# Optimization experiments

Measured on AMD Instinct MI355X. Metric: run time of the kernel, lower is better.

The kernel has to match this reference:

```python
import jax, jax.numpy as jnp
import numpy as np

HID, HEADS, LAYERS = 64, 4, 2
D = HID // HEADS
NU, NE, NV = 30000, 60000, 1000
N_NODES = (NU, NE, NV)
OFFS = (0, NU, NU + NE, NU + NE + NV)
N_TOTAL = NU + NE + NV
# (src_type, dst_type, n_edges); node types: user=0, event=1, venue=2. Order matches module.edge_types.
EDGE_DEFS = (
    (0, 0, 150000),  # friend
    (0, 1, 120000), (0, 1, 60000), (0, 1, 40000), (0, 1, 30000), (0, 1, 50000),  # view/like/save/intent/attend
    (1, 0, 120000), (1, 0, 60000), (1, 0, 40000), (1, 0, 30000), (1, 0, 50000),  # rev_*
    (1, 2, 60000),  # hosted_at
    (2, 1, 60000),  # hosts
)
EDGE_NAMES = ('ei_friend', 'ei_view', 'ei_like', 'ei_save', 'ei_intent', 'ei_attend',
              'ei_rev_view', 'ei_rev_like', 'ei_rev_save', 'ei_rev_intent', 'ei_rev_attend',
              'ei_hosted_at', 'ei_hosts')


def _l2norm(x):
    return x / jnp.maximum(jnp.linalg.norm(x, axis=-1, keepdims=True), 1e-12)


def _hgt_layer(h, edges, Wkqv, bkqv, Wk, Wv, p_rel, Wout, bout, skip):
    # h: list of per-node-type features [N_t, HID]. Fused K/Q/V projection per node type.
    kqv = [h[t] @ Wkqv[t] + bkqv[t] for t in range(3)]  # [N_t, 3*HID]
    k = [a[:, :HID].reshape(-1, HEADS, D) for a in kqv]
    q = [a[:, HID:2 * HID].reshape(-1, HEADS, D) for a in kqv]
    v = [a[:, 2 * HID:].reshape(-1, HEADS, D) for a in kqv]
    scale = 1.0 / np.sqrt(D).astype(np.float32)
    scores, msgs, dsts = [], [], []
    for e, (s, d, _) in enumerate(EDGE_DEFS):
        src_idx, dst_idx = edges[e][0], edges[e][1]
        # per-(edge_type, head) DxD relation transforms (PyG k_rel / v_rel)
        ke = jnp.einsum('nhd,hde->nhe', k[s], Wk[e])[src_idx]  # [E,H,D]
        ve = jnp.einsum('nhd,hde->nhe', v[s], Wv[e])[src_idx]  # [E,H,D]
        qi = q[d][dst_idx]                                      # [E,H,D]
        scores.append((qi * ke).sum(-1) * p_rel[e] * scale)     # [E,H]
        msgs.append(ve)
        dsts.append(dst_idx + OFFS[d])
    sc = jnp.concatenate(scores)   # [E_tot, H]
    ms = jnp.concatenate(msgs)     # [E_tot, H, D]
    dst = jnp.concatenate(dsts)    # [E_tot] global destination ids
    # destination-grouped softmax across all edge types jointly
    smax = jax.lax.stop_gradient(jax.ops.segment_max(sc, dst, num_segments=N_TOTAL))
    ex = jnp.exp(sc - smax[dst])
    den = jax.ops.segment_sum(ex, dst, num_segments=N_TOTAL)
    alpha = ex / den[dst]
    agg = jax.ops.segment_sum(alpha[:, :, None] * ms, dst, num_segments=N_TOTAL).reshape(N_TOTAL, HID)
    out = []
    for t in range(3):
        o = agg[OFFS[t]:OFFS[t + 1]]
        a = jax.nn.gelu(o, approximate=False) @ Wout[t] + bout[t]
        g = jax.nn.sigmoid(skip[t])  # learnable skip gate
        out.append(g * a + (1.0 - g) * h[t])
    return out


def _forward(x_user, x_event, x_venue, W_user, b_user, W_event, b_event, W_venue, b_venue,
             emb_user, emb_event, emb_venue, Wkqv, bkqv, Wk, Wv, p_rel, Wout, bout, skip,
             ids_user, ids_event, ids_venue, edges):
    h = [x_user @ W_user + b_user + emb_user[ids_user],
         x_event @ W_event + b_event + emb_event[ids_event],
         x_venue @ W_venue + b_venue + emb_venue[ids_venue]]
    for l in range(LAYERS):
        h = _hgt_layer(h, edges, Wkqv[l], bkqv[l], Wk[l], Wv[l], p_rel[l], Wout[l], bout[l], skip[l])
        h = [jax.nn.relu(x) for x in h]  # dropout is identity in eval mode
    return tuple(_l2norm(x) for x in h)


def setup_inputs() -> dict:
    key = jax.random.key(0)
    ks = iter(jax.random.split(key, 64))
    s = 0.05
    inp = {
        'x_user': jax.random.normal(next(ks), (NU, 32), jnp.float32),
        'x_event': jax.random.normal(next(ks), (NE, 32), jnp.float32),
        'x_venue': jax.random.normal(next(ks), (NV, 16), jnp.float32),
        'W_user': jax.random.normal(next(ks), (32, HID), jnp.float32) * s,
        'b_user': jnp.zeros((HID,), jnp.float32),
        'W_event': jax.random.normal(next(ks), (32, HID), jnp.float32) * s,
        'b_event': jnp.zeros((HID,), jnp.float32),
        'W_venue': jax.random.normal(next(ks), (16, HID), jnp.float32) * s,
        'b_venue': jnp.zeros((HID,), jnp.float32),
        'emb_user': jax.random.normal(next(ks), (NU, HID), jnp.float32) * s,
        'emb_event': jax.random.normal(next(ks), (NE, HID), jnp.float32) * s,
        'emb_venue': jax.random.normal(next(ks), (NV, HID), jnp.float32) * s,
        'Wkqv': jax.random.normal(next(ks), (LAYERS, 3, HID, 3 * HID), jnp.float32) * s,
        'bkqv': jnp.zeros((LAYERS, 3, 3 * HID), jnp.float32),
        'Wk': jax.random.normal(next(ks), (LAYERS, 13, HEADS, D, D), jnp.float32) * 0.2,
        'Wv': jax.random.normal(next(ks), (LAYERS, 13, HEADS, D, D), jnp.float32) * 0.2,
        'p_rel': jnp.ones((LAYERS, 13, HEADS), jnp.float32),
        'Wout': jax.random.normal(next(ks), (LAYERS, 3, HID, HID), jnp.float32) * s,
        'bout': jnp.zeros((LAYERS, 3, HID), jnp.float32),
        'skip': jnp.ones((LAYERS, 3), jnp.float32),
        'ids_user': jnp.arange(NU, dtype=jnp.int32),
        'ids_event': jnp.arange(NE, dtype=jnp.int32),
        'ids_venue': jnp.arange(NV, dtype=jnp.int32),
    }
    for name, (st, dt, n) in zip(EDGE_NAMES, EDGE_DEFS):
        src = jax.random.randint(next(ks), (n,), 0, N_NODES[st], dtype=jnp.int32)
        dst = jax.random.randint(next(ks), (n,), 0, N_NODES[dt], dtype=jnp.int32)
        inp[name] = jnp.stack([src, dst])
    return inp


def reference(x_user, x_event, x_venue, W_user, b_user, W_event, b_event, W_venue, b_venue,
              emb_user, emb_event, emb_venue, Wkqv, bkqv, Wk, Wv, p_rel, Wout, bout, skip,
              ids_user, ids_event, ids_venue,
              ei_friend, ei_view, ei_like, ei_save, ei_intent, ei_attend,
              ei_rev_view, ei_rev_like, ei_rev_save, ei_rev_intent, ei_rev_attend,
              ei_hosted_at, ei_hosts):
    edges = (ei_friend, ei_view, ei_like, ei_save, ei_intent, ei_attend,
             ei_rev_view, ei_rev_like, ei_rev_save, ei_rev_intent, ei_rev_attend,
             ei_hosted_at, ei_hosts)
    return _forward(x_user, x_event, x_venue, W_user, b_user, W_event, b_event, W_venue, b_venue,
                    emb_user, emb_event, emb_venue, Wkqv, bkqv, Wk, Wv, p_rel, Wout, bout, skip,
                    ids_user, ids_event, ids_venue, edges)
```

## Files before the change

kernel.cpp:

```cpp
#include <hip/hip_runtime.h>
#include <hip/hip_fp16.h>
#include <math.h>

#define HID   64
#define HEADS 4
#define DH    16
#define NU    30000
#define NE_   60000
#define NV    1000
#define NTOT  91000
#define ETOT  870000
#define NSLOT 541000
#define LAYERS 2

__device__ const int d_EOFF[14] = {0,150000,270000,330000,370000,400000,450000,
                                   570000,630000,670000,700000,750000,810000,870000};
__device__ const int d_ECNT[13] = {150000,120000,60000,40000,30000,50000,
                                   120000,60000,40000,30000,50000,60000,60000};
__device__ const int d_EST[13]  = {0,0,0,0,0,0,1,1,1,1,1,1,2};
__device__ const int d_EDT[13]  = {0,1,1,1,1,1,0,0,0,0,0,2,1};
__device__ const int d_NOFF[3]  = {0, NU, NU + NE_};
__device__ const int d_EBASE[13] = {0,30000,60000,90000,120000,150000,
                                    180000,240000,300000,360000,420000,480000,540000};

struct EdgePtrs { const int* p[13]; };

typedef float f32x2 __attribute__((ext_vector_type(2)));

__device__ __forceinline__ void pk_fma(f32x2& acc, f32x2 a, f32x2 b) {
    asm("v_pk_fma_f32 %0, %1, %2, %0" : "+v"(acc) : "v"(a), "v"(b));
}
__device__ __forceinline__ void pk_fma_sv(f32x2& acc, f32x2 a_sgpr, f32x2 b) {
    asm("v_pk_fma_f32 %0, %1, %2, %0" : "+v"(acc) : "s"(a_sgpr), "v"(b));
}

__device__ __forceinline__ int node_type(int n) {
    return (n >= NU) + (n >= NU + NE_);
}

__global__ __launch_bounds__(64)
void k_init(const float* __restrict__ xu, const float* __restrict__ xe,
            const float* __restrict__ xv,
            const float* __restrict__ Wu, const float* __restrict__ bu,
            const float* __restrict__ We, const float* __restrict__ be,
            const float* __restrict__ Wv_, const float* __restrict__ bv,
            const float* __restrict__ embu, const float* __restrict__ embe,
            const float* __restrict__ embv,
            const int* __restrict__ idu, const int* __restrict__ ide,
            const int* __restrict__ idv,
            float* __restrict__ h) {
    int n0 = blockIdx.x * 16;
    int t = node_type(n0);
    int j = threadIdx.x;
    const float *x, *W, *bb, *emb; const int* ids; int in_dim;
    if (t == 0)      { x = xu; W = Wu;  bb = bu; emb = embu; ids = idu; in_dim = 32; }
    else if (t == 1) { x = xe; W = We;  bb = be; emb = embe; ids = ide; in_dim = 32; }
    else             { x = xv; W = Wv_; bb = bv; emb = embv; ids = idv; in_dim = 16; }
    int nl = n0 - d_NOFF[t];
    int nn = min(16, NTOT - n0);
    __shared__ float xT[32][20];
    int ncs = (in_dim == 32) ? 3 : 2;
    int nch = 1 << ncs;
    for (int idx = j; idx < (nch << 4); idx += 64) {
        int n = idx >> ncs, c = idx & (nch - 1);
        float4 v = make_float4(0.f, 0.f, 0.f, 0.f);
        if (n < nn) v = *(const float4*)(x + (size_t)(nl + n) * in_dim + c * 4);
        xT[c * 4 + 0][n] = v.x;
        xT[c * 4 + 1][n] = v.y;
        xT[c * 4 + 2][n] = v.z;
        xT[c * 4 + 3][n] = v.w;
    }
    __syncthreads();
    float bj = bb[j];
    f32x2 acc2[8];
    #pragma unroll
    for (int p = 0; p < 8; p++) {
        float ex = (2 * p     < nn) ? emb[(size_t)ids[nl + 2 * p    ] * 64 + j] : 0.f;
        float ey = (2 * p + 1 < nn) ? emb[(size_t)ids[nl + 2 * p + 1] * 64 + j] : 0.f;
        acc2[p].x = bj + ex; acc2[p].y = bj + ey;
    }
    if (in_dim == 32) {
        #pragma unroll
        for (int i = 0; i < 32; i++) {
            float w = W[i * 64 + j];
            f32x2 w2; w2.x = w; w2.y = w;
            #pragma unroll
            for (int qd = 0; qd < 4; qd++) {
                float4 hv = *(const float4*)(&xT[i][qd * 4]);
                f32x2 p0; p0.x = hv.x; p0.y = hv.y; pk_fma(acc2[2 * qd],     p0, w2);
                f32x2 p1; p1.x = hv.z; p1.y = hv.w; pk_fma(acc2[2 * qd + 1], p1, w2);
            }
        }
    } else {
        #pragma unroll
        for (int i = 0; i < 16; i++) {
            float w = W[i * 64 + j];
            f32x2 w2; w2.x = w; w2.y = w;
            #pragma unroll
            for (int qd = 0; qd < 4; qd++) {
                float4 hv = *(const float4*)(&xT[i][qd * 4]);
                f32x2 p0; p0.x = hv.x; p0.y = hv.y; pk_fma(acc2[2 * qd],     p0, w2);
                f32x2 p1; p1.x = hv.z; p1.y = hv.w; pk_fma(acc2[2 * qd + 1], p1, w2);
            }
        }
    }
    #pragma unroll
    for (int p = 0; p < 8; p++) {
        if (2 * p     < nn) h[(size_t)(n0 + 2 * p)     * 64 + j] = acc2[p].x;
        if (2 * p + 1 < nn) h[(size_t)(n0 + 2 * p + 1) * 64 + j] = acc2[p].y;
    }
}

__global__ void k_cnt(EdgePtrs ep, int* __restrict__ cnt, int* __restrict__ pos) {
    int eidx = blockIdx.x * blockDim.x + threadIdx.x;
    if (eidx >= ETOT) return;
    int e = 0;
    #pragma unroll
    for (int i = 1; i < 13; i++) e += (eidx >= d_EOFF[i]);
    int li = eidx - d_EOFF[e];
    int dst = ep.p[e][d_ECNT[e] + li];
    pos[eidx] = atomicAdd(&cnt[d_NOFF[d_EDT[e]] + dst], 1);
}

__global__ void k_scan_a(const int* __restrict__ cnt, int* __restrict__ partial) {
    __shared__ int s[256];
    int i = blockIdx.x * 256 + threadIdx.x;
    s[threadIdx.x] = (i < NTOT) ? cnt[i] : 0;
    __syncthreads();
    for (int off = 128; off > 0; off >>= 1) {
        if (threadIdx.x < off) s[threadIdx.x] += s[threadIdx.x + off];
        __syncthreads();
    }
    if (threadIdx.x == 0) partial[blockIdx.x] = s[0];
}

__global__ void k_scan_b(int* __restrict__ partial, int nblk) {
    __shared__ int s[512];
    int t = threadIdx.x;
    s[t] = (t < nblk) ? partial[t] : 0;
    __syncthreads();
    for (int off = 1; off < 512; off <<= 1) {
        int v = (t >= off) ? s[t - off] : 0;
        __syncthreads();
        s[t] += v;
        __syncthreads();
    }
    if (t < nblk) partial[t] = t ? s[t - 1] : 0;
}

__global__ void k_scan_c(const int* __restrict__ cnt, const int* __restrict__ partial,
                         int* __restrict__ row_ptr) {
    __shared__ int s[256];
    int i = blockIdx.x * 256 + threadIdx.x, t = threadIdx.x;
    int v = (i < NTOT) ? cnt[i] : 0;
    s[t] = v;
    __syncthreads();
    for (int off = 1; off < 256; off <<= 1) {
        int u = (t >= off) ? s[t - off] : 0;
        __syncthreads();
        s[t] += u;
        __syncthreads();
    }
    if (i < NTOT) row_ptr[i] = s[t] - v + partial[blockIdx.x];
    if (i == NTOT - 1) row_ptr[NTOT] = s[t] + partial[blockIdx.x];
}

__global__ void k_fill(EdgePtrs ep, const int* __restrict__ row_ptr,
                       const int* __restrict__ pos, int* __restrict__ csr) {
    int eidx = blockIdx.x * blockDim.x + threadIdx.x;
    if (eidx >= ETOT) return;
    int e = 0;
    #pragma unroll
    for (int i = 1; i < 13; i++) e += (eidx >= d_EOFF[i]);
    int li = eidx - d_EOFF[e];
    const int* base = ep.p[e];
    int src = base[li], dst = base[d_ECNT[e] + li];
    int dg = d_NOFF[d_EDT[e]] + dst;
    csr[row_ptr[dg] + pos[eidx]] = d_EBASE[e] + src;
}

__global__ __launch_bounds__(192, 3)
void k_kqvt(const float* __restrict__ h, const float* __restrict__ Wkqv,
            const float* __restrict__ bkqv, const float* __restrict__ Wk,
            const float* __restrict__ Wv, const float* __restrict__ prel,
            float* __restrict__ qagg, __half2* __restrict__ kvt, int layer) {
    int n0 = blockIdx.x * 16;
    int t = node_type(n0);
    __shared__ float kq[16][192];
    int j = threadIdx.x;

    const float* hb = h + (size_t)n0 * 64;
    const float* Wc = Wkqv + (size_t)(layer * 3 + t) * HID * 192 + j;
    float b = bkqv[(layer * 3 + t) * 192 + j];
    f32x2 acc2[16];
    #pragma unroll
    for (int n = 0; n < 16; n++) { acc2[n].x = 0.f; acc2[n].y = 0.f; }
    #pragma unroll
    for (int ic = 0; ic < 16; ic++) {
        float w0 = Wc[(size_t)(4 * ic + 0) * 192];
        float w1 = Wc[(size_t)(4 * ic + 1) * 192];
        float w2 = Wc[(size_t)(4 * ic + 2) * 192];
        float w3 = Wc[(size_t)(4 * ic + 3) * 192];
        f32x2 wA; wA.x = w0; wA.y = w1;
        f32x2 wB; wB.x = w2; wB.y = w3;
        #pragma unroll
        for (int n = 0; n < 16; n++) {
            float4 hv = *(const float4*)(hb + n * 64 + ic * 4);
            f32x2 p0; p0.x = hv.x; p0.y = hv.y;
            pk_fma_sv(acc2[n], p0, wA);
            f32x2 p1; p1.x = hv.z; p1.y = hv.w;
            pk_fma_sv(acc2[n], p1, wB);
        }
    }
    float accf[16];
    #pragma unroll
    for (int n = 0; n < 16; n++) accf[n] = b + acc2[n].x + acc2[n].y;
    #pragma unroll
    for (int n = 0; n < 16; n++) kq[n][j] = accf[n];
    if (j >= 64 && j < 128) {
        #pragma unroll
        for (int n = 0; n < 16; n++)
            if (n0 + n < NTOT) qagg[(size_t)(n0 + n) * 64 + (j - 64)] = accf[n];
    }
    __syncthreads();

    int wave = j >> 6, lane = j & 63;
    int hh = lane >> 4, xo = lane & 15;
    int ne = (t == 2) ? 1 : 6;
    int e0 = (t == 0) ? 0 : (t == 1) ? 6 : 12;
    int eA = e0 + wave, eB = e0 + wave + 3;
    bool vA = wave < ne, vB = wave + 3 < ne;
    int nt = n0 - d_NOFF[t];
    f32x2 wkA[8], wvA[8], wkB[8], wvB[8];
    int sbA = 0, sbB = 0;
    if (vA) {
        const float* Wkp = Wk + (((size_t)layer * 13 + eA) * 4 + hh) * 256 + xo;
        const float* Wvp = Wv + (((size_t)layer * 13 + eA) * 4 + hh) * 256 + xo;
        float pr = prel[(layer * 13 + eA) * 4 + hh] * 0.25f;
        #pragma unroll
        for (int p = 0; p < 8; p++) {
            wkA[p].x = Wkp[(2 * p)     * 16] * pr;
            wkA[p].y = Wkp[(2 * p + 1) * 16] * pr;
            wvA[p].x = Wvp[(2 * p)     * 16];
            wvA[p].y = Wvp[(2 * p + 1) * 16];
        }
        sbA = d_EBASE[eA] + nt;
    }
    if (vB) {
        const float* Wkp = Wk + (((size_t)layer * 13 + eB) * 4 + hh) * 256 + xo;
        const float* Wvp = Wv + (((size_t)layer * 13 + eB) * 4 + hh) * 256 + xo;
        float pr = prel[(layer * 13 + eB) * 4 + hh] * 0.25f;
        #pragma unroll
        for (int p = 0; p < 8; p++) {
            wkB[p].x = Wkp[(2 * p)     * 16] * pr;
            wkB[p].y = Wkp[(2 * p + 1) * 16] * pr;
            wvB[p].x = Wvp[(2 * p)     * 16];
            wvB[p].y = Wvp[(2 * p + 1) * 16];
        }
        sbB = d_EBASE[eB] + nt;
    }
    #pragma unroll
    for (int n = 0; n < 16; n++) {
        bool ok = (n0 + n) < NTOT;
        const float* kr = &kq[n][hh * 16];
        const float* vr = &kq[n][128 + hh * 16];
        float4 k0 = ((const float4*)kr)[0];
        float4 k1 = ((const float4*)kr)[1];
        float4 k2 = ((const float4*)kr)[2];
        float4 k3 = ((const float4*)kr)[3];
        float4 v0 = ((const float4*)vr)[0];
        float4 v1 = ((const float4*)vr)[1];
        float4 v2 = ((const float4*)vr)[2];
        float4 v3 = ((const float4*)vr)[3];
        if (vA & ok) {
            f32x2 ak; ak.x = 0.f; ak.y = 0.f;
            f32x2 av; av.x = 0.f; av.y = 0.f;
            f32x2 p0;
            p0.x = k0.x; p0.y = k0.y; pk_fma(ak, p0, wkA[0]);
            p0.x = k0.z; p0.y = k0.w; pk_fma(ak, p0, wkA[1]);
            p0.x = k1.x; p0.y = k1.y; pk_fma(ak, p0, wkA[2]);
            p0.x = k1.z; p0.y = k1.w; pk_fma(ak, p0, wkA[3]);
            p0.x = k2.x; p0.y = k2.y; pk_fma(ak, p0, wkA[4]);
            p0.x = k2.z; p0.y = k2.w; pk_fma(ak, p0, wkA[5]);
            p0.x = k3.x; p0.y = k3.y; pk_fma(ak, p0, wkA[6]);
            p0.x = k3.z; p0.y = k3.w; pk_fma(ak, p0, wkA[7]);
            p0.x = v0.x; p0.y = v0.y; pk_fma(av, p0, wvA[0]);
            p0.x = v0.z; p0.y = v0.w; pk_fma(av, p0, wvA[1]);
            p0.x = v1.x; p0.y = v1.y; pk_fma(av, p0, wvA[2]);
            p0.x = v1.z; p0.y = v1.w; pk_fma(av, p0, wvA[3]);
            p0.x = v2.x; p0.y = v2.y; pk_fma(av, p0, wvA[4]);
            p0.x = v2.z; p0.y = v2.w; pk_fma(av, p0, wvA[5]);
            p0.x = v3.x; p0.y = v3.y; pk_fma(av, p0, wvA[6]);
            p0.x = v3.z; p0.y = v3.w; pk_fma(av, p0, wvA[7]);
            float kt = ak.x + ak.y;
            float vt = av.x + av.y;
            kvt[(size_t)(sbA + n) * 64 + lane] = __float22half2_rn(make_float2(kt, vt));
        }
        if (vB & ok) {
            f32x2 ak; ak.x = 0.f; ak.y = 0.f;
            f32x2 av; av.x = 0.f; av.y = 0.f;
            f32x2 p0;
            p0.x = k0.x; p0.y = k0.y; pk_fma(ak, p0, wkB[0]);
            p0.x = k0.z; p0.y = k0.w; pk_fma(ak, p0, wkB[1]);
            p0.x = k1.x; p0.y = k1.y; pk_fma(ak, p0, wkB[2]);
            p0.x = k1.z; p0.y = k1.w; pk_fma(ak, p0, wkB[3]);
            p0.x = k2.x; p0.y = k2.y; pk_fma(ak, p0, wkB[4]);
            p0.x = k2.z; p0.y = k2.w; pk_fma(ak, p0, wkB[5]);
            p0.x = k3.x; p0.y = k3.y; pk_fma(ak, p0, wkB[6]);
            p0.x = k3.z; p0.y = k3.w; pk_fma(ak, p0, wkB[7]);
            p0.x = v0.x; p0.y = v0.y; pk_fma(av, p0, wvB[0]);
            p0.x = v0.z; p0.y = v0.w; pk_fma(av, p0, wvB[1]);
            p0.x = v1.x; p0.y = v1.y; pk_fma(av, p0, wvB[2]);
            p0.x = v1.z; p0.y = v1.w; pk_fma(av, p0, wvB[3]);
            p0.x = v2.x; p0.y = v2.y; pk_fma(av, p0, wvB[4]);
            p0.x = v2.z; p0.y = v2.w; pk_fma(av, p0, wvB[5]);
            p0.x = v3.x; p0.y = v3.y; pk_fma(av, p0, wvB[6]);
            p0.x = v3.z; p0.y = v3.w; pk_fma(av, p0, wvB[7]);
            float kt = ak.x + ak.y;
            float vt = av.x + av.y;
            kvt[(size_t)(sbB + n) * 64 + lane] = __float22half2_rn(make_float2(kt, vt));
        }
    }
}

__device__ __forceinline__ float row_sum16(float x) {
    int v;
    v = __builtin_amdgcn_update_dpp(0, __float_as_int(x), 0xB1, 0xF, 0xF, true);
    x += __int_as_float(v);
    v = __builtin_amdgcn_update_dpp(0, __float_as_int(x), 0x4E, 0xF, 0xF, true);
    x += __int_as_float(v);
    v = __builtin_amdgcn_update_dpp(0, __float_as_int(x), 0x141, 0xF, 0xF, true);
    x += __int_as_float(v);
    v = __builtin_amdgcn_update_dpp(0, __float_as_int(x), 0x140, 0xF, 0xF, true);
    x += __int_as_float(v);
    return x;
}

__device__ __forceinline__ void osm_step(float s, float vv,
                                         float& m, float& l, float& acc) {
    float d = s - m;
    float t = __expf(-fabsf(d));
    bool pos = d > 0.f;
    m = fmaxf(m, s);
    float sc = pos ? t : 1.f;
    float es = pos ? 1.f : t;
    l   = l * sc + es;
    acc = acc * sc + es * vv;
}

__global__ __launch_bounds__(512, 8)
void k_gather(float* __restrict__ qagg, const __half2* __restrict__ kvt,
              const int* __restrict__ row_ptr, const int* __restrict__ csr) {
    int wave = threadIdx.x >> 6, lane = threadIdx.x & 63;
    int node = blockIdx.x * 8 + wave;
    if (node >= NTOT) return;
    float q = qagg[(size_t)node * 64 + lane];
    int beg = row_ptr[node], end = row_ptr[node + 1];
    float m0 = -1e30f, l0 = 0.f, a0 = 0.f;
    float m1 = -1e30f, l1 = 0.f, a1 = 0.f;
    float m2 = -1e30f, l2 = 0.f, a2 = 0.f;
    float m3 = -1e30f, l3 = 0.f, a3 = 0.f;
    for (int base = beg; base < end; base += 64) {
        int n = end - base; if (n > 64) n = 64;
        int ent = csr[base + ((lane < n) ? lane : 0)];
        for (int c = 0; c < n; c += 8) {
            int cn = n - c; if (cn > 8) cn = 8;
            __half2 f[8];
            #pragma unroll
            for (int k = 0; k < 8; k++) {
                int idx = c + ((k < cn) ? k : 0);
                int sl = __shfl(ent, idx, 64);
                f[k] = kvt[(size_t)sl * 64 + lane];
            }
            float s8[8];
            #pragma unroll
            for (int k = 0; k < 8; k++) {
                if (k >= cn) break;
                s8[k] = row_sum16(q * __low2float(f[k]));
            }
            if (0 < cn) osm_step(s8[0], __high2float(f[0]), m0, l0, a0);
            if (1 < cn) osm_step(s8[1], __high2float(f[1]), m1, l1, a1);
            if (2 < cn) osm_step(s8[2], __high2float(f[2]), m2, l2, a2);
            if (3 < cn) osm_step(s8[3], __high2float(f[3]), m3, l3, a3);
            if (4 < cn) osm_step(s8[4], __high2float(f[4]), m0, l0, a0);
            if (5 < cn) osm_step(s8[5], __high2float(f[5]), m1, l1, a1);
            if (6 < cn) osm_step(s8[6], __high2float(f[6]), m2, l2, a2);
            if (7 < cn) osm_step(s8[7], __high2float(f[7]), m3, l3, a3);
        }
    }
    float M   = fmaxf(fmaxf(m0, m1), fmaxf(m2, m3));
    float e0  = __expf(m0 - M), e1 = __expf(m1 - M);
    float e2  = __expf(m2 - M), e3 = __expf(m3 - M);
    float l   = l0 * e0 + l1 * e1 + l2 * e2 + l3 * e3;
    float acc = a0 * e0 + a1 * e1 + a2 * e2 + a3 * e3;
    qagg[(size_t)node * 64 + lane] = (l > 0.f) ? acc / l : 0.f;
}

__global__ __launch_bounds__(256)
void k_out(const float* __restrict__ agg, const float* __restrict__ Wout,
           const float* __restrict__ bout, const float* __restrict__ skip,
           float* __restrict__ h, float* __restrict__ out, int layer, int last) {
    int b = blockIdx.x; int t, n0, lim;
    if (b < 938)       { t = 0; n0 = b * 32;                 lim = NU; }
    else if (b < 2813) { t = 1; n0 = NU + (b - 938) * 32;    lim = NU + NE_; }
    else               { t = 2; n0 = NU + NE_ + (b - 2813) * 32; lim = NTOT; }
    int nn = min(32, lim - n0);
    __shared__ float gsT[64][36];
    for (int i = threadIdx.x; i < nn * 64; i += 256) {
        float o = agg[(size_t)n0 * 64 + i];
        gsT[i & 63][i >> 6] = 0.5f * o * (1.f + erff(o * 0.70710678118654752f));
    }
    __syncthreads();
    int j = threadIdx.x & 63, g = threadIdx.x >> 6;
    const float* W = Wout + (size_t)(layer * 3 + t) * HID * HID;
    float bb = bout[(layer * 3 + t) * HID + j];
    f32x2 acc2[4];
    #pragma unroll
    for (int p = 0; p < 4; p++) { acc2[p].x = bb; acc2[p].y = bb; }
    for (int i = 0; i < 64; i++) {
        float w = W[i * 64 + j];
        f32x2 w2; w2.x = w; w2.y = w;
        float4 a = *(const float4*)(&gsT[i][g * 8]);
        float4 c = *(const float4*)(&gsT[i][g * 8 + 4]);
        f32x2 p0; p0.x = a.x; p0.y = a.y; pk_fma(acc2[0], p0, w2);
        f32x2 p1; p1.x = a.z; p1.y = a.w; pk_fma(acc2[1], p1, w2);
        f32x2 p2; p2.x = c.x; p2.y = c.y; pk_fma(acc2[2], p2, w2);
        f32x2 p3; p3.x = c.z; p3.y = c.w; pk_fma(acc2[3], p3, w2);
    }
    float acc[8];
    #pragma unroll
    for (int p = 0; p < 4; p++) { acc[2 * p] = acc2[p].x; acc[2 * p + 1] = acc2[p].y; }
    float gk = 1.f / (1.f + __expf(-skip[layer * 3 + t]));
    #pragma unroll
    for (int n = 0; n < 8; n++) {
        int node = n0 + g * 8 + n;
        if (node >= lim) continue;
        float r = gk * acc[n] + (1.f - gk) * h[(size_t)node * 64 + j];
        r = fmaxf(r, 0.f);
        if (!last) {
            h[(size_t)node * 64 + j] = r;
        } else {
            float ss = r * r;
            ss += __shfl_xor(ss, 1, 64);  ss += __shfl_xor(ss, 2, 64);
            ss += __shfl_xor(ss, 4, 64);  ss += __shfl_xor(ss, 8, 64);
            ss += __shfl_xor(ss, 16, 64); ss += __shfl_xor(ss, 32, 64);
            float nrm = fmaxf(sqrtf(ss), 1e-12f);
            out[(size_t)node * 64 + j] = r / nrm;
        }
    }
}

extern "C" void kernel_launch(void* const* d_in, const int* in_sizes, int n_in,
                              void* d_out, int out_size, void* d_ws, size_t ws_size,
                              hipStream_t stream) {
    const float* xu   = (const float*)d_in[0];
    const float* xe   = (const float*)d_in[1];
    const float* xv   = (const float*)d_in[2];
    const float* Wu   = (const float*)d_in[3];
    const float* bu   = (const float*)d_in[4];
    const float* We   = (const float*)d_in[5];
    const float* be   = (const float*)d_in[6];
    const float* Wv_  = (const float*)d_in[7];
    const float* bv   = (const float*)d_in[8];
    const float* embu = (const float*)d_in[9];
    const float* embe = (const float*)d_in[10];
    const float* embv = (const float*)d_in[11];
    const float* Wkqv = (const float*)d_in[12];
    const float* bkqv = (const float*)d_in[13];
    const float* Wk   = (const float*)d_in[14];
    const float* Wv   = (const float*)d_in[15];
    const float* prel = (const float*)d_in[16];
    const float* Wout = (const float*)d_in[17];
    const float* bout = (const float*)d_in[18];
    const float* skip = (const float*)d_in[19];
    const int*   idu  = (const int*)d_in[20];
    const int*   ide  = (const int*)d_in[21];
    const int*   idv  = (const int*)d_in[22];
    EdgePtrs ep;
    for (int e = 0; e < 13; e++) ep.p[e] = (const int*)d_in[23 + e];

    float* ws  = (float*)d_ws;
    float* h      = ws;
    float* qagg   = h    + (size_t)NTOT * HID;
    __half2* kvt  = (__half2*)(qagg + (size_t)NTOT * HID);
    int* cnt     = (int*)(kvt + (size_t)NSLOT * HID);
    int* row_ptr = cnt + NTOT;
    int* partial = row_ptr + NTOT + 1;
    int* csr     = partial + 512;
    int* pos     = csr + ETOT;

    k_init<<<(NTOT + 15) / 16, 64, 0, stream>>>(
        xu, xe, xv, Wu, bu, We, be, Wv_, bv, embu, embe, embv, idu, ide, idv, h);

    hipMemsetAsync(cnt, 0, (size_t)NTOT * 4, stream);
    int nblk = (NTOT + 255) / 256;
    k_cnt<<<(ETOT + 255) / 256, 256, 0, stream>>>(ep, cnt, pos);
    k_scan_a<<<nblk, 256, 0, stream>>>(cnt, partial);
    k_scan_b<<<1, 512, 0, stream>>>(partial, nblk);
    k_scan_c<<<nblk, 256, 0, stream>>>(cnt, partial, row_ptr);
    k_fill<<<(ETOT + 255) / 256, 256, 0, stream>>>(ep, row_ptr, pos, csr);

    for (int l = 0; l < LAYERS; l++) {
        k_kqvt<<<(NTOT + 15) / 16, 192, 0, stream>>>(h, Wkqv, bkqv, Wk, Wv, prel,
                                                     qagg, kvt, l);
        k_gather<<<(NTOT + 7) / 8, 512, 0, stream>>>(qagg, kvt, row_ptr, csr);
        k_out<<<2845, 256, 0, stream>>>(qagg, Wout, bout, skip, h,
                                        (float*)d_out, l, l == LAYERS - 1);
    }
}
```

Before: 598.9 us.

## Fuse output projection, GELU and skip gate into the gather kernel

```diff
diff --git a/kernel.cpp b/kernel.cpp
--- a/kernel.cpp
+++ b/kernel.cpp
@@ -348,12 +348,19 @@
     acc = acc * sc + es * vv;
 }
 
-__global__ __launch_bounds__(512, 8)
-void k_gather(float* __restrict__ qagg, const __half2* __restrict__ kvt,
-              const int* __restrict__ row_ptr, const int* __restrict__ csr) {
+__global__ __launch_bounds__(512, 4)
+void k_gather(const float* __restrict__ qagg, const __half2* __restrict__ kvt,
+              const int* __restrict__ row_ptr, const int* __restrict__ csr,
+              const float* __restrict__ Wout, const float* __restrict__ bout,
+              const float* __restrict__ skip,
+              float* __restrict__ h, float* __restrict__ out,
+              int layer, int last) {
     int wave = threadIdx.x >> 6, lane = threadIdx.x & 63;
     int node = blockIdx.x * 8 + wave;
-    if (node >= NTOT) return;
+    int t = node_type(node);
+    float hprev = h[(size_t)node * 64 + lane];
+    float bb = bout[(layer * 3 + t) * 64 + lane];
+    float gk = 1.f / (1.f + __expf(-skip[layer * 3 + t]));
     float q = qagg[(size_t)node * 64 + lane];
     int beg = row_ptr[node], end = row_ptr[node + 1];
     float m0 = -1e30f, l0 = 0.f, a0 = 0.f;
@@ -393,60 +400,39 @@
     float e2  = __expf(m2 - M), e3 = __expf(m3 - M);
     float l   = l0 * e0 + l1 * e1 + l2 * e2 + l3 * e3;
     float acc = a0 * e0 + a1 * e1 + a2 * e2 + a3 * e3;
-    qagg[(size_t)node * 64 + lane] = (l > 0.f) ? acc / l : 0.f;
-}
-
-__global__ __launch_bounds__(256)
-void k_out(const float* __restrict__ agg, const float* __restrict__ Wout,
-           const float* __restrict__ bout, const float* __restrict__ skip,
-           float* __restrict__ h, float* __restrict__ out, int layer, int last) {
-    int b = blockIdx.x; int t, n0, lim;
-    if (b < 938)       { t = 0; n0 = b * 32;                 lim = NU; }
-    else if (b < 2813) { t = 1; n0 = NU + (b - 938) * 32;    lim = NU + NE_; }
-    else               { t = 2; n0 = NU + NE_ + (b - 2813) * 32; lim = NTOT; }
-    int nn = min(32, lim - n0);
-    __shared__ float gsT[64][36];
-    for (int i = threadIdx.x; i < nn * 64; i += 256) {
-        float o = agg[(size_t)n0 * 64 + i];
-        gsT[i & 63][i >> 6] = 0.5f * o * (1.f + erff(o * 0.70710678118654752f));
-    }
-    __syncthreads();
-    int j = threadIdx.x & 63, g = threadIdx.x >> 6;
-    const float* W = Wout + (size_t)(layer * 3 + t) * HID * HID;
-    float bb = bout[(layer * 3 + t) * HID + j];
-    f32x2 acc2[4];
-    #pragma unroll
-    for (int p = 0; p < 4; p++) { acc2[p].x = bb; acc2[p].y = bb; }
-    for (int i = 0; i < 64; i++) {
-        float w = W[i * 64 + j];
-        f32x2 w2; w2.x = w; w2.y = w;
-        float4 a = *(const float4*)(&gsT[i][g * 8]);
-        float4 c = *(const float4*)(&gsT[i][g * 8 + 4]);
-        f32x2 p0; p0.x = a.x; p0.y = a.y; pk_fma(acc2[0], p0, w2);
-        f32x2 p1; p1.x = a.z; p1.y = a.w; pk_fma(acc2[1], p1, w2);
-        f32x2 p2; p2.x = c.x; p2.y = c.y; pk_fma(acc2[2], p2, w2);
-        f32x2 p3; p3.x = c.z; p3.y = c.w; pk_fma(acc2[3], p3, w2);
-    }
-    float acc[8];
-    #pragma unroll
-    for (int p = 0; p < 4; p++) { acc[2 * p] = acc2[p].x; acc[2 * p + 1] = acc2[p].y; }
-    float gk = 1.f / (1.f + __expf(-skip[layer * 3 + t]));
-    #pragma unroll
-    for (int n = 0; n < 8; n++) {
-        int node = n0 + g * 8 + n;
-        if (node >= lim) continue;
-        float r = gk * acc[n] + (1.f - gk) * h[(size_t)node * 64 + j];
-        r = fmaxf(r, 0.f);
-        if (!last) {
-            h[(size_t)node * 64 + j] = r;
-        } else {
-            float ss = r * r;
-            ss += __shfl_xor(ss, 1, 64);  ss += __shfl_xor(ss, 2, 64);
-            ss += __shfl_xor(ss, 4, 64);  ss += __shfl_xor(ss, 8, 64);
-            ss += __shfl_xor(ss, 16, 64); ss += __shfl_xor(ss, 32, 64);
-            float nrm = fmaxf(sqrtf(ss), 1e-12f);
-            out[(size_t)node * 64 + j] = r / nrm;
-        }
+    float og  = (l > 0.f) ? acc / l : 0.f;
+
+    float gl = 0.5f * og * (1.f + erff(og * 0.70710678118654752f));
+    __shared__ float gs[8][64];
+    gs[wave][lane] = gl;
+    const float* W = Wout + (size_t)(layer * 3 + t) * 4096 + lane;
+    const float* gsp = &gs[wave][0];
+    f32x2 a2v; a2v.x = bb; a2v.y = 0.f;
+    #pragma unroll
+    for (int i4 = 0; i4 < 16; i4++) {
+        float4 g4 = *(const float4*)(gsp + i4 * 4);
+        float w0 = W[(size_t)(i4 * 4 + 0) * 64];
+        float w1 = W[(size_t)(i4 * 4 + 1) * 64];
+        float w2 = W[(size_t)(i4 * 4 + 2) * 64];
+        float w3 = W[(size_t)(i4 * 4 + 3) * 64];
+        f32x2 p0; p0.x = g4.x; p0.y = g4.y;
+        f32x2 q0; q0.x = w0;  q0.y = w1;
+        pk_fma(a2v, p0, q0);
+        f32x2 p1; p1.x = g4.z; p1.y = g4.w;
+        f32x2 q1; q1.x = w2;  q1.y = w3;
+        pk_fma(a2v, p1, q1);
+    }
+    float r = gk * (a2v.x + a2v.y) + (1.f - gk) * hprev;
+    r = fmaxf(r, 0.f);
+    if (!last) {
+        h[(size_t)node * 64 + lane] = r;
+    } else {
+        float ss = r * r;
+        ss += __shfl_xor(ss, 1, 64);  ss += __shfl_xor(ss, 2, 64);
+        ss += __shfl_xor(ss, 4, 64);  ss += __shfl_xor(ss, 8, 64);
+        ss += __shfl_xor(ss, 16, 64); ss += __shfl_xor(ss, 32, 64);
+        float nrm = fmaxf(sqrtf(ss), 1e-12f);
+        out[(size_t)node * 64 + lane] = r / nrm;
     }
 }
 
@@ -503,8 +489,8 @@
     for (int l = 0; l < LAYERS; l++) {
         k_kqvt<<<(NTOT + 15) / 16, 192, 0, stream>>>(h, Wkqv, bkqv, Wk, Wv, prel,
                                                      qagg, kvt, l);
-        k_gather<<<(NTOT + 7) / 8, 512, 0, stream>>>(qagg, kvt, row_ptr, csr);
-        k_out<<<2845, 256, 0, stream>>>(qagg, Wout, bout, skip, h,
-                                        (float*)d_out, l, l == LAYERS - 1);
-    }
-}
+        k_gather<<<NTOT / 8, 512, 0, stream>>>(qagg, kvt, row_ptr, csr,
+                                               Wout, bout, skip, h,
+                                               (float*)d_out, l, l == LAYERS - 1);
+    }
+}
```

Result: slower. 628.2 us (+4.9%).
